# Kernel optimization log

Hardware: AMD Instinct MI355X
Metric: run time of the kernel (lower is better)

The kernel has to match this reference:

```python
import jax, jax.numpy as jnp
import numpy as np

NUM_NODES = 65536      # 16 graphs x 4096 nodes
NODES_PER_GRAPH = 4096
NUM_GRAPHS = 16
NUM_EDGES = 1048576    # avg degree 16
DIM = 64


def setup_inputs() -> dict:
    key = jax.random.key(0)
    ks = jax.random.split(key, 10)
    # edges constrained within each component graph (batched-graph semantics)
    eper = NUM_EDGES // NUM_GRAPHS
    gid = np.repeat(np.arange(NUM_GRAPHS), eper)
    rng = np.random.default_rng(0)
    src = jnp.asarray(rng.integers(0, NODES_PER_GRAPH, NUM_EDGES) + gid * NODES_PER_GRAPH, dtype=jnp.int64)
    dst = jnp.asarray(rng.integers(0, NODES_PER_GRAPH, NUM_EDGES) + gid * NODES_PER_GRAPH, dtype=jnp.int64)
    s = 1.0 / np.sqrt(DIM)
    return {
        "x": jax.random.normal(ks[0], (NUM_NODES, DIM), dtype=jnp.float32),
        "W1": jax.random.normal(ks[1], (DIM, DIM), dtype=jnp.float32) * s,
        "b1": jnp.zeros((DIM,), dtype=jnp.float32),
        "W2": jax.random.normal(ks[2], (DIM, DIM), dtype=jnp.float32) * s,
        "b2": jnp.zeros((DIM,), dtype=jnp.float32),
        "W3": jax.random.normal(ks[3], (DIM, DIM), dtype=jnp.float32) * s,
        "b3": jnp.zeros((DIM,), dtype=jnp.float32),
        "src": src,
        "dst": dst,
        "num_graphs": NUM_GRAPHS,
    }


def _sym_norms(src, dst, n):
    ones = jnp.ones(src.shape[0], dtype=jnp.float32)
    deg_out = jax.ops.segment_sum(ones, src, num_segments=n)
    deg_in = jax.ops.segment_sum(ones, dst, num_segments=n)
    inv_sqrt = lambda d: jnp.where(d > 0, d, 1.0) ** -0.5 * (d > 0)
    return inv_sqrt(deg_out), inv_sqrt(deg_in)


def _graph_conv(x, W, b, src, dst, norm_src, norm_dst, n):
    # DGL GraphConv, norm='both': h = D_in^{-1/2} A D_out^{-1/2} (X W) + b
    h = (x * norm_src[:, None]) @ W          # [N, D]
    msg = h[src]                              # [E, D] gather
    agg = jax.ops.segment_sum(msg, dst, num_segments=n)  # [N, D] scatter-add
    return agg * norm_dst[:, None] + b


def reference(x, W1, b1, W2, b2, W3, b3, src, dst, num_graphs):
    n = x.shape[0]
    norm_src, norm_dst = _sym_norms(src, dst, n)
    h = _graph_conv(x, W1, b1, src, dst, norm_src, norm_dst, n)
    h = _graph_conv(h, W2, b2, src, dst, norm_src, norm_dst, n)
    h = _graph_conv(h, W3, b3, src, dst, norm_src, norm_dst, n)
    # unbatch + pad to max_num_nodes + stack; equal-size graphs -> pure reshape
    return h.reshape(num_graphs, n // num_graphs, h.shape[-1])
```

## Files before the change

### kernel.cpp

```cpp
#include <hip/hip_runtime.h>
#include <hip/hip_fp16.h>

#define DIM 64
#define NG  16
#define CPG 16
#define NPG 4096
#define LSTR 68
#define HISTB (NG*CPG)
#define GGN 32

__global__ __launch_bounds__(256) void kA_hist(
    const int* __restrict__ src, const int* __restrict__ dst,
    int* __restrict__ hsub, int* __restrict__ dsub, int chunk, int npg)
{
    __shared__ int hs[NPG], hd[NPG];
    const int blk = blockIdx.x;
    const int g = blk / CPG;
    const int t = threadIdx.x;
    const int ebase = blk * chunk;
    const int nbase = g * npg;
    for (int i = t; i < npg; i += 256) { hs[i] = 0; hd[i] = 0; }
    __syncthreads();
    for (int e = t; e < chunk; e += 256) {
        atomicAdd(&hs[src[ebase + e] - nbase], 1);
        atomicAdd(&hd[dst[ebase + e] - nbase], 1);
    }
    __syncthreads();
    for (int i = t; i < npg; i += 256) {
        hsub[blk * npg + i] = hs[i];
        hd[i] ? (dsub[blk * npg + i] = hd[i]) : (dsub[blk * npg + i] = 0);
    }
}

__global__ __launch_bounds__(1024) void k2_scan(
    const int* __restrict__ hsub, int* __restrict__ dsub,
    float* __restrict__ ns, float* __restrict__ nd,
    int* __restrict__ rowptr, int epg, int npg, int N, int E)
{
    __shared__ int ddeg[NPG];
    __shared__ int wsum[16];
    const int g = blockIdx.x;
    const int t = threadIdx.x;
    const int nbase = g * npg;
    const int ebase = g * epg;
    for (int i = t; i < npg; i += 1024) {
        int sd = 0, dd = 0;
#pragma unroll
        for (int k = 0; k < CPG; ++k) {
            sd += hsub[(g * CPG + k) * npg + i];
            dd += dsub[(g * CPG + k) * npg + i];
        }
        ns[nbase + i] = sd > 0 ? rsqrtf((float)sd) : 0.0f;
        nd[nbase + i] = dd > 0 ? rsqrtf((float)dd) : 0.0f;
        ddeg[i] = dd;
    }
    __syncthreads();
    const int i0 = 4 * t;
    int d0 = ddeg[i0], d1 = ddeg[i0 + 1], d2 = ddeg[i0 + 2], d3 = ddeg[i0 + 3];
    int s4 = d0 + d1 + d2 + d3;
    const int lane = t & 63, wid = t >> 6;
    int v = s4;
#pragma unroll
    for (int off = 1; off < 64; off <<= 1) {
        int u = __shfl_up(v, off, 64);
        if (lane >= off) v += u;
    }
    if (lane == 63) wsum[wid] = v;
    __syncthreads();
    if (t < 16) {
        int w = wsum[t];
#pragma unroll
        for (int off = 1; off < 16; off <<= 1) {
            int u = __shfl_up(w, off, 16);
            if (t >= off) w += u;
        }
        wsum[t] = w;
    }
    __syncthreads();
    int incl = v + (wid > 0 ? wsum[wid - 1] : 0);
    int c = ebase + incl - s4;
    rowptr[nbase + i0    ] = c; ddeg[i0    ] = c; c += d0;
    rowptr[nbase + i0 + 1] = c; ddeg[i0 + 1] = c; c += d1;
    rowptr[nbase + i0 + 2] = c; ddeg[i0 + 2] = c; c += d2;
    rowptr[nbase + i0 + 3] = c; ddeg[i0 + 3] = c;
    if (g == 0 && t == 0) rowptr[N] = E;
    __syncthreads();
    for (int i = t; i < npg; i += 1024) {
        int cc = ddeg[i];
#pragma unroll
        for (int k = 0; k < CPG; ++k) {
            int* p = &dsub[(g * CPG + k) * npg + i];
            int old = *p; *p = cc; cc += old;
        }
    }
}

__global__ __launch_bounds__(256) void kC_gemm_fill(
    const int* __restrict__ src, const int* __restrict__ dst,
    const int* __restrict__ dsub, int* __restrict__ ssrc, int chunk, int npg,
    const float* __restrict__ x, const float* __restrict__ W1,
    const float* __restrict__ ns, __half* __restrict__ hF, int swiz)
{
    __shared__ float smem[64 * LSTR + 32 * LSTR];
    const int tid = threadIdx.x;
    if ((int)blockIdx.x < HISTB) {
        int* cur = (int*)smem;
        const int blk = blockIdx.x;
        const int g = blk / CPG;
        const int ebase = blk * chunk;
        const int nbase = g * npg;
        for (int i = tid; i < npg; i += 256) cur[i] = dsub[blk * npg + i];
        __syncthreads();
        for (int e = tid; e < chunk; e += 256) {
            int s = src[ebase + e];
            int d = dst[ebase + e] - nbase;
            int pos = atomicAdd(&cur[d], 1);
            ssrc[pos] = s;
        }
    } else {
        float* Wt = smem;
        float* xs = Wt + 64 * LSTR;
        int blk = blockIdx.x - HISTB;
        if (swiz) {
            int xg = blk & 7;
            int j = blk >> 3;
            int g = xg + ((j >> 7) << 3);
            blk = (g << 7) + (j & 127);
        }
        const int row0 = blk * 32;
        for (int i = tid; i < 64 * 64; i += 256) {
            int k = i >> 6, c = i & 63;
            Wt[c * LSTR + k] = W1[i];
        }
        for (int i = tid; i < 32 * 64; i += 256) {
            int r = i >> 6, c = i & 63;
            int row = row0 + r;
            xs[r * LSTR + c] = x[(size_t)row * 64 + c] * ns[row];
        }
        __syncthreads();
        const int c0 = tid & 31;
        const int r0 = tid >> 5;
        float acc[4][2] = {};
#pragma unroll
        for (int k = 0; k < 64; k += 4) {
            float4 w0 = *(const float4*)&Wt[(c0     ) * LSTR + k];
            float4 w1 = *(const float4*)&Wt[(c0 + 32) * LSTR + k];
#pragma unroll
            for (int rr = 0; rr < 4; ++rr) {
                float4 xv = *(const float4*)&xs[(r0 + 8 * rr) * LSTR + k];
                acc[rr][0] += xv.x * w0.x + xv.y * w0.y + xv.z * w0.z + xv.w * w0.w;
                acc[rr][1] += xv.x * w1.x + xv.y * w1.y + xv.z * w1.z + xv.w * w1.w;
            }
        }
#pragma unroll
        for (int rr = 0; rr < 4; ++rr) {
            int row = row0 + r0 + 8 * rr;
            hF[(size_t)row * 64 + c0     ] = __float2half_rn(acc[rr][0]);
            hF[(size_t)row * 64 + c0 + 32] = __float2half_rn(acc[rr][1]);
        }
    }
}

__device__ __forceinline__ void acc_h4(float4& acc, uint2 u)
{
    __half2 p = *(__half2*)&u.x;
    __half2 q = *(__half2*)&u.y;
    float2 f0 = __half22float2(p);
    float2 f1 = __half22float2(q);
    acc.x += f0.x; acc.y += f0.y; acc.z += f1.x; acc.w += f1.y;
}

__device__ __forceinline__ void acc_h4s(float4& acc, uint2 u, float s)
{
    __half2 p = *(__half2*)&u.x;
    __half2 q = *(__half2*)&u.y;
    float2 f0 = __half22float2(p);
    float2 f1 = __half22float2(q);
    acc.x += s * f0.x; acc.y += s * f0.y; acc.z += s * f1.x; acc.w += s * f1.y;
}

__device__ __forceinline__ void gather_rest(
    const __half* __restrict__ h, const int* __restrict__ ssrc,
    int j, int end, int sub, float4& acc)
{
    const size_t off = (size_t)sub * 4;
    const int last = end - 8;
    while (j <= last) {
        int s0 = ssrc[j+0], s1 = ssrc[j+1], s2 = ssrc[j+2], s3 = ssrc[j+3];
        int s4 = ssrc[j+4], s5 = ssrc[j+5], s6 = ssrc[j+6], s7 = ssrc[j+7];
        uint2 u0 = *(const uint2*)(h + (size_t)s0 * 64 + off);
        uint2 u1 = *(const uint2*)(h + (size_t)s1 * 64 + off);
        uint2 u2 = *(const uint2*)(h + (size_t)s2 * 64 + off);
        uint2 u3 = *(const uint2*)(h + (size_t)s3 * 64 + off);
        uint2 u4 = *(const uint2*)(h + (size_t)s4 * 64 + off);
        uint2 u5 = *(const uint2*)(h + (size_t)s5 * 64 + off);
        uint2 u6 = *(const uint2*)(h + (size_t)s6 * 64 + off);
        uint2 u7 = *(const uint2*)(h + (size_t)s7 * 64 + off);
        acc_h4(acc, u0); acc_h4(acc, u1); acc_h4(acc, u2); acc_h4(acc, u3);
        acc_h4(acc, u4); acc_h4(acc, u5); acc_h4(acc, u6); acc_h4(acc, u7);
        j += 8;
    }
    int rem = end - j;
    if (rem > 0) {
#pragma unroll
        for (int q = 0; q < 4; ++q) {
            int jj = j + (q < rem ? q : rem - 1);
            int s = ssrc[jj];
            uint2 u = *(const uint2*)(h + (size_t)s * 64 + off);
            acc_h4s(acc, u, (q < rem) ? 1.0f : 0.0f);
        }
        if (rem > 4) {
#pragma unroll
            for (int q = 4; q < 8; ++q) {
                int jj = j + (q < rem ? q : rem - 1);
                int s = ssrc[jj];
                uint2 u = *(const uint2*)(h + (size_t)s * 64 + off);
                acc_h4s(acc, u, (q < rem) ? 1.0f : 0.0f);
            }
        }
    }
}

__device__ __forceinline__ void gather_node2(
    const __half* __restrict__ h, const int* __restrict__ ssrc,
    int begA, int endA, int begB, int endB, int sub,
    float4& accA, float4& accB)
{
    const size_t off = (size_t)sub * 4;
    int jA = begA, jB = begB;
    const int lastA = endA - 8, lastB = endB - 8;
    if (jA <= lastA && jB <= lastB) {
        int a0 = ssrc[jA+0], a1 = ssrc[jA+1], a2 = ssrc[jA+2], a3 = ssrc[jA+3];
        int a4 = ssrc[jA+4], a5 = ssrc[jA+5], a6 = ssrc[jA+6], a7 = ssrc[jA+7];
        int b0 = ssrc[jB+0], b1 = ssrc[jB+1], b2 = ssrc[jB+2], b3 = ssrc[jB+3];
        int b4 = ssrc[jB+4], b5 = ssrc[jB+5], b6 = ssrc[jB+6], b7 = ssrc[jB+7];
        for (;;) {
            uint2 uA0 = *(const uint2*)(h + (size_t)a0 * 64 + off);
            uint2 uA1 = *(const uint2*)(h + (size_t)a1 * 64 + off);
            uint2 uA2 = *(const uint2*)(h + (size_t)a2 * 64 + off);
            uint2 uA3 = *(const uint2*)(h + (size_t)a3 * 64 + off);
            uint2 uA4 = *(const uint2*)(h + (size_t)a4 * 64 + off);
            uint2 uA5 = *(const uint2*)(h + (size_t)a5 * 64 + off);
            uint2 uA6 = *(const uint2*)(h + (size_t)a6 * 64 + off);
            uint2 uA7 = *(const uint2*)(h + (size_t)a7 * 64 + off);
            uint2 uB0 = *(const uint2*)(h + (size_t)b0 * 64 + off);
            uint2 uB1 = *(const uint2*)(h + (size_t)b1 * 64 + off);
            uint2 uB2 = *(const uint2*)(h + (size_t)b2 * 64 + off);
            uint2 uB3 = *(const uint2*)(h + (size_t)b3 * 64 + off);
            uint2 uB4 = *(const uint2*)(h + (size_t)b4 * 64 + off);
            uint2 uB5 = *(const uint2*)(h + (size_t)b5 * 64 + off);
            uint2 uB6 = *(const uint2*)(h + (size_t)b6 * 64 + off);
            uint2 uB7 = *(const uint2*)(h + (size_t)b7 * 64 + off);
            jA += 8; jB += 8;
            bool more = (jA <= lastA) && (jB <= lastB);
            int pA = more ? jA : begA;
            int pB = more ? jB : begB;
            int na0 = ssrc[pA+0], na1 = ssrc[pA+1], na2 = ssrc[pA+2], na3 = ssrc[pA+3];
            int na4 = ssrc[pA+4], na5 = ssrc[pA+5], na6 = ssrc[pA+6], na7 = ssrc[pA+7];
            int nb0 = ssrc[pB+0], nb1 = ssrc[pB+1], nb2 = ssrc[pB+2], nb3 = ssrc[pB+3];
            int nb4 = ssrc[pB+4], nb5 = ssrc[pB+5], nb6 = ssrc[pB+6], nb7 = ssrc[pB+7];
            acc_h4(accA, uA0); acc_h4(accA, uA1); acc_h4(accA, uA2); acc_h4(accA, uA3);
            acc_h4(accA, uA4); acc_h4(accA, uA5); acc_h4(accA, uA6); acc_h4(accA, uA7);
            acc_h4(accB, uB0); acc_h4(accB, uB1); acc_h4(accB, uB2); acc_h4(accB, uB3);
            acc_h4(accB, uB4); acc_h4(accB, uB5); acc_h4(accB, uB6); acc_h4(accB, uB7);
            if (!more) break;
            a0 = na0; a1 = na1; a2 = na2; a3 = na3;
            a4 = na4; a5 = na5; a6 = na6; a7 = na7;
            b0 = nb0; b1 = nb1; b2 = nb2; b3 = nb3;
            b4 = nb4; b5 = nb5; b6 = nb6; b7 = nb7;
        }
    }
    gather_rest(h, ssrc, jA, endA, sub, accA);
    gather_rest(h, ssrc, jB, endB, sub, accB);
}

__global__ __launch_bounds__(256) void gg_kernel(
    const __half* __restrict__ h, const int* __restrict__ ssrc,
    const int* __restrict__ rowptr, const float* __restrict__ ns,
    const float* __restrict__ nd, const float* __restrict__ bprev,
    const float* __restrict__ W, __half* __restrict__ hout,
    int N, int swiz)
{
    __shared__ float us[GGN][64];
    int blk = blockIdx.x;
    if (swiz) {
        int xg = blk & 7;
        int j = blk >> 3;
        int g = xg + ((j >> 7) << 3);
        blk = (g << 7) + (j & 127);
    }
    const int tid = threadIdx.x;
    const int wv = tid >> 6;
    const int lane = tid & 63;
    const int grp = lane >> 4;
    const int sub = lane & 15;

    const int nlA = wv * 4 + grp;
    const int nlB = nlA + 16;
    const int wA = blk * GGN + nlA;
    const int wB = blk * GGN + nlB;
    {
        int begA = rowptr[wA], endA = rowptr[wA + 1];
        int begB = rowptr[wB], endB = rowptr[wB + 1];
        float4 accA = {0.f,0.f,0.f,0.f}, accB = {0.f,0.f,0.f,0.f};
        gather_node2(h, ssrc, begA, endA, begB, endB, sub, accA, accB);
        float4 bv = *(const float4*)(bprev + sub * 4);
        {
            float sw = ns[wA];
            float alpha = nd[wA] * sw;
            float4 uo;
            uo.x = accA.x * alpha + sw * bv.x;
            uo.y = accA.y * alpha + sw * bv.y;
            uo.z = accA.z * alpha + sw * bv.z;
            uo.w = accA.w * alpha + sw * bv.w;
            *(float4*)&us[nlA][sub * 4] = uo;
        }
        {
            float sw = ns[wB];
            float alpha = nd[wB] * sw;
            float4 uo;
            uo.x = accB.x * alpha + sw * bv.x;
            uo.y = accB.y * alpha + sw * bv.y;
            uo.z = accB.z * alpha + sw * bv.z;
            uo.w = accB.w * alpha + sw * bv.w;
            *(float4*)&us[nlB][sub * 4] = uo;
        }
    }
    __syncthreads();
    const int c = tid & 63;
    const int nb = tid >> 6;
    float y[8] = {0.f,0.f,0.f,0.f,0.f,0.f,0.f,0.f};
#pragma unroll
    for (int k = 0; k < 64; k += 4) {
        float w0 = W[(k    ) * 64 + c];
        float w1 = W[(k + 1) * 64 + c];
        float w2 = W[(k + 2) * 64 + c];
        float w3 = W[(k + 3) * 64 + c];
#pragma unroll
        for (int m = 0; m < 8; ++m) {
            const float4 uv = *(const float4*)&us[nb + 4 * m][k];
            y[m] += uv.x * w0 + uv.y * w1 + uv.z * w2 + uv.w * w3;
        }
    }
#pragma unroll
    for (int m = 0; m < 8; ++m) {
        int wo = blk * GGN + nb + 4 * m;
        hout[(size_t)wo * 64 + c] = __float2half_rn(y[m]);
    }
}

__global__ __launch_bounds__(256) void gather_kernel(
    const __half* __restrict__ h, const int* __restrict__ ssrc,
    const int* __restrict__ rowptr, float* __restrict__ out,
    const float* __restrict__ nd, const float* __restrict__ b,
    int N, int swiz)
{
    int blk = blockIdx.x;
    if (swiz) {
        int x = blk & 7;
        int j = blk >> 3;
        int g = x + ((j >> 7) << 3);
        blk = (g << 7) + (j & 127);
    }
    const int wv = threadIdx.x >> 6;
    const int lane = threadIdx.x & 63;
    const int grp = lane >> 4;
    const int sub = lane & 15;
    int wA = blk * 32 + wv * 4 + grp;
    int wB = wA + 16;
    int begA = rowptr[wA], endA = rowptr[wA + 1];
    int begB = rowptr[wB], endB = rowptr[wB + 1];
    float4 accA = {0.f,0.f,0.f,0.f}, accB = {0.f,0.f,0.f,0.f};
    gather_node2(h, ssrc, begA, endA, begB, endB, sub, accA, accB);
    const float4 bv = *(const float4*)(b + sub * 4);
    {
        float n = nd[wA];
        accA.x = accA.x * n + bv.x;
        accA.y = accA.y * n + bv.y;
        accA.z = accA.z * n + bv.z;
        accA.w = accA.w * n + bv.w;
        *(float4*)(out + (size_t)wA * 64 + sub * 4) = accA;
    }
    {
        float n = nd[wB];
        accB.x = accB.x * n + bv.x;
        accB.y = accB.y * n + bv.y;
        accB.z = accB.z * n + bv.z;
        accB.w = accB.w * n + bv.w;
        *(float4*)(out + (size_t)wB * 64 + sub * 4) = accB;
    }
}

extern "C" void kernel_launch(void* const* d_in, const int* in_sizes, int n_in,
                              void* d_out, int out_size, void* d_ws, size_t ws_size,
                              hipStream_t stream)
{
    const float* x  = (const float*)d_in[0];
    const float* W1 = (const float*)d_in[1];
    const float* b1 = (const float*)d_in[2];
    const float* W2 = (const float*)d_in[3];
    const float* b2 = (const float*)d_in[4];
    const float* W3 = (const float*)d_in[5];
    const float* b3 = (const float*)d_in[6];
    const int*  src = (const int*)d_in[7];
    const int*  dst = (const int*)d_in[8];

    const int E = in_sizes[7];
    const int N = in_sizes[0] / DIM;
    const int epg = E / NG;
    const int npg = N / NG;
    const int chunk = epg / CPG;

    float*  ns     = (float*)d_ws;
    float*  nd     = ns + N;
    __half* hF     = (__half*)(nd + N);
    __half* h2     = hF + (size_t)N * DIM;
    int*    rowptr = (int*)(h2 + (size_t)N * DIM);
    int*    ssrc   = rowptr + N + 1;
    int*    hsub   = ssrc + E;
    int*    dsub   = hsub + (size_t)HISTB * npg;
    float*  agg    = (float*)d_out;

    const int swiz = (N == 65536 && npg == 4096) ? 1 : 0;

    kA_hist<<<HISTB, 256, 0, stream>>>(src, dst, hsub, dsub, chunk, npg);
    k2_scan<<<NG, 1024, 0, stream>>>(
        hsub, dsub, ns, nd, rowptr, epg, npg, N, E);
    kC_gemm_fill<<<HISTB + N / 32, 256, 0, stream>>>(
        src, dst, dsub, ssrc, chunk, npg, x, W1, ns, hF, swiz);

    gg_kernel<<<N / GGN, 256, 0, stream>>>(
        hF, ssrc, rowptr, ns, nd, b1, W2, h2, N, swiz);
    gg_kernel<<<N / GGN, 256, 0, stream>>>(
        h2, ssrc, rowptr, ns, nd, b2, W3, hF, N, swiz);
    gather_kernel<<<N / 32, 256, 0, stream>>>(
        hF, ssrc, rowptr, agg, nd, b3, N, swiz);
}
```

Before: 213.2 us.

## Split degree scan into parallel kernels and widen gather to 16-byte loads

The single 16-block scan kernel becomes three kernels. Two of them are fully parallel, one computing norms and destination degrees and one computing per-chunk cursors, with a small scan between them, so the serial per-graph loops no longer run on only 16 blocks. The gather kernels now use 8 lanes per node with 16-byte half loads instead of 16 lanes with 8-byte loads. The gather-GEMM tile doubles to 64 nodes per block, with the swizzle adjusted to match. This trades two extra launches and the extra degd buffer for more parallelism, and the wider loads cut the number of load instructions in the gather, though there are fewer lanes per row.

```diff
diff --git a/kernel.cpp b/kernel.cpp
--- a/kernel.cpp
+++ b/kernel.cpp
@@ -7,7 +7,7 @@
 #define NPG 4096
 #define LSTR 68
 #define HISTB (NG*CPG)
-#define GGN 32
+#define GGN 64
 
 __global__ __launch_bounds__(256) void kA_hist(
     const int* __restrict__ src, const int* __restrict__ dst,
@@ -28,36 +28,41 @@
     __syncthreads();
     for (int i = t; i < npg; i += 256) {
         hsub[blk * npg + i] = hs[i];
-        hd[i] ? (dsub[blk * npg + i] = hd[i]) : (dsub[blk * npg + i] = 0);
-    }
-}
-
-__global__ __launch_bounds__(1024) void k2_scan(
-    const int* __restrict__ hsub, int* __restrict__ dsub,
-    float* __restrict__ ns, float* __restrict__ nd,
-    int* __restrict__ rowptr, int epg, int npg, int N, int E)
-{
-    __shared__ int ddeg[NPG];
+        dsub[blk * npg + i] = hd[i];
+    }
+}
+
+__global__ __launch_bounds__(256) void k2a_norms(
+    const int* __restrict__ hsub, const int* __restrict__ dsub,
+    float* __restrict__ ns, float* __restrict__ nd, int* __restrict__ degd,
+    int npg)
+{
+    const int node = blockIdx.x * 256 + threadIdx.x;
+    const int g = node / npg;
+    const int i = node - g * npg;
+    int sd = 0, dd = 0;
+#pragma unroll
+    for (int k = 0; k < CPG; ++k) {
+        sd += hsub[(g * CPG + k) * npg + i];
+        dd += dsub[(g * CPG + k) * npg + i];
+    }
+    ns[node] = sd > 0 ? rsqrtf((float)sd) : 0.0f;
+    nd[node] = dd > 0 ? rsqrtf((float)dd) : 0.0f;
+    degd[node] = dd;
+}
+
+__global__ __launch_bounds__(1024) void k2b_scan(
+    const int* __restrict__ degd, int* __restrict__ rowptr,
+    int epg, int npg, int N, int E)
+{
     __shared__ int wsum[16];
     const int g = blockIdx.x;
     const int t = threadIdx.x;
     const int nbase = g * npg;
     const int ebase = g * epg;
-    for (int i = t; i < npg; i += 1024) {
-        int sd = 0, dd = 0;
-#pragma unroll
-        for (int k = 0; k < CPG; ++k) {
-            sd += hsub[(g * CPG + k) * npg + i];
-            dd += dsub[(g * CPG + k) * npg + i];
-        }
-        ns[nbase + i] = sd > 0 ? rsqrtf((float)sd) : 0.0f;
-        nd[nbase + i] = dd > 0 ? rsqrtf((float)dd) : 0.0f;
-        ddeg[i] = dd;
-    }
-    __syncthreads();
     const int i0 = 4 * t;
-    int d0 = ddeg[i0], d1 = ddeg[i0 + 1], d2 = ddeg[i0 + 2], d3 = ddeg[i0 + 3];
-    int s4 = d0 + d1 + d2 + d3;
+    const int4 d = *(const int4*)&degd[nbase + i0];
+    int s4 = d.x + d.y + d.z + d.w;
     const int lane = t & 63, wid = t >> 6;
     int v = s4;
 #pragma unroll
@@ -79,19 +84,24 @@
     __syncthreads();
     int incl = v + (wid > 0 ? wsum[wid - 1] : 0);
     int c = ebase + incl - s4;
-    rowptr[nbase + i0    ] = c; ddeg[i0    ] = c; c += d0;
-    rowptr[nbase + i0 + 1] = c; ddeg[i0 + 1] = c; c += d1;
-    rowptr[nbase + i0 + 2] = c; ddeg[i0 + 2] = c; c += d2;
-    rowptr[nbase + i0 + 3] = c; ddeg[i0 + 3] = c;
+    rowptr[nbase + i0    ] = c; c += d.x;
+    rowptr[nbase + i0 + 1] = c; c += d.y;
+    rowptr[nbase + i0 + 2] = c; c += d.z;
+    rowptr[nbase + i0 + 3] = c;
     if (g == 0 && t == 0) rowptr[N] = E;
-    __syncthreads();
-    for (int i = t; i < npg; i += 1024) {
-        int cc = ddeg[i];
-#pragma unroll
-        for (int k = 0; k < CPG; ++k) {
-            int* p = &dsub[(g * CPG + k) * npg + i];
-            int old = *p; *p = cc; cc += old;
-        }
+}
+
+__global__ __launch_bounds__(256) void k2c_cursors(
+    int* __restrict__ dsub, const int* __restrict__ rowptr, int npg)
+{
+    const int node = blockIdx.x * 256 + threadIdx.x;
+    const int g = node / npg;
+    const int i = node - g * npg;
+    int cc = rowptr[node];
+#pragma unroll
+    for (int k = 0; k < CPG; ++k) {
+        int* p = &dsub[(g * CPG + k) * npg + i];
+        int old = *p; *p = cc; cc += old;
     }
 }
 
@@ -161,43 +171,49 @@
     }
 }
 
-__device__ __forceinline__ void acc_h4(float4& acc, uint2 u)
-{
-    __half2 p = *(__half2*)&u.x;
-    __half2 q = *(__half2*)&u.y;
-    float2 f0 = __half22float2(p);
-    float2 f1 = __half22float2(q);
-    acc.x += f0.x; acc.y += f0.y; acc.z += f1.x; acc.w += f1.y;
-}
-
-__device__ __forceinline__ void acc_h4s(float4& acc, uint2 u, float s)
-{
-    __half2 p = *(__half2*)&u.x;
-    __half2 q = *(__half2*)&u.y;
-    float2 f0 = __half22float2(p);
-    float2 f1 = __half22float2(q);
-    acc.x += s * f0.x; acc.y += s * f0.y; acc.z += s * f1.x; acc.w += s * f1.y;
+__device__ __forceinline__ void acc_u4(float4& A, float4& B, uint4 u)
+{
+    __half2 h0 = *(__half2*)&u.x;
+    __half2 h1 = *(__half2*)&u.y;
+    __half2 h2 = *(__half2*)&u.z;
+    __half2 h3 = *(__half2*)&u.w;
+    float2 f0 = __half22float2(h0), f1 = __half22float2(h1);
+    float2 f2 = __half22float2(h2), f3 = __half22float2(h3);
+    A.x += f0.x; A.y += f0.y; A.z += f1.x; A.w += f1.y;
+    B.x += f2.x; B.y += f2.y; B.z += f3.x; B.w += f3.y;
+}
+
+__device__ __forceinline__ void acc_u4s(float4& A, float4& B, uint4 u, float s)
+{
+    __half2 h0 = *(__half2*)&u.x;
+    __half2 h1 = *(__half2*)&u.y;
+    __half2 h2 = *(__half2*)&u.z;
+    __half2 h3 = *(__half2*)&u.w;
+    float2 f0 = __half22float2(h0), f1 = __half22float2(h1);
+    float2 f2 = __half22float2(h2), f3 = __half22float2(h3);
+    A.x += s * f0.x; A.y += s * f0.y; A.z += s * f1.x; A.w += s * f1.y;
+    B.x += s * f2.x; B.y += s * f2.y; B.z += s * f3.x; B.w += s * f3.y;
 }
 
 __device__ __forceinline__ void gather_rest(
     const __half* __restrict__ h, const int* __restrict__ ssrc,
-    int j, int end, int sub, float4& acc)
-{
-    const size_t off = (size_t)sub * 4;
+    int j, int end, int sub, float4& A, float4& B)
+{
+    const size_t off = (size_t)sub * 8;
     const int last = end - 8;
     while (j <= last) {
         int s0 = ssrc[j+0], s1 = ssrc[j+1], s2 = ssrc[j+2], s3 = ssrc[j+3];
         int s4 = ssrc[j+4], s5 = ssrc[j+5], s6 = ssrc[j+6], s7 = ssrc[j+7];
-        uint2 u0 = *(const uint2*)(h + (size_t)s0 * 64 + off);
-        uint2 u1 = *(const uint2*)(h + (size_t)s1 * 64 + off);
-        uint2 u2 = *(const uint2*)(h + (size_t)s2 * 64 + off);
-        uint2 u3 = *(const uint2*)(h + (size_t)s3 * 64 + off);
-        uint2 u4 = *(const uint2*)(h + (size_t)s4 * 64 + off);
-        uint2 u5 = *(const uint2*)(h + (size_t)s5 * 64 + off);
-        uint2 u6 = *(const uint2*)(h + (size_t)s6 * 64 + off);
-        uint2 u7 = *(const uint2*)(h + (size_t)s7 * 64 + off);
-        acc_h4(acc, u0); acc_h4(acc, u1); acc_h4(acc, u2); acc_h4(acc, u3);
-        acc_h4(acc, u4); acc_h4(acc, u5); acc_h4(acc, u6); acc_h4(acc, u7);
+        uint4 u0 = *(const uint4*)(h + (size_t)s0 * 64 + off);
+        uint4 u1 = *(const uint4*)(h + (size_t)s1 * 64 + off);
+        uint4 u2 = *(const uint4*)(h + (size_t)s2 * 64 + off);
+        uint4 u3 = *(const uint4*)(h + (size_t)s3 * 64 + off);
+        uint4 u4 = *(const uint4*)(h + (size_t)s4 * 64 + off);
+        uint4 u5 = *(const uint4*)(h + (size_t)s5 * 64 + off);
+        uint4 u6 = *(const uint4*)(h + (size_t)s6 * 64 + off);
+        uint4 u7 = *(const uint4*)(h + (size_t)s7 * 64 + off);
+        acc_u4(A, B, u0); acc_u4(A, B, u1); acc_u4(A, B, u2); acc_u4(A, B, u3);
+        acc_u4(A, B, u4); acc_u4(A, B, u5); acc_u4(A, B, u6); acc_u4(A, B, u7);
         j += 8;
     }
     int rem = end - j;
@@ -206,16 +222,16 @@
         for (int q = 0; q < 4; ++q) {
             int jj = j + (q < rem ? q : rem - 1);
             int s = ssrc[jj];
-            uint2 u = *(const uint2*)(h + (size_t)s * 64 + off);
-            acc_h4s(acc, u, (q < rem) ? 1.0f : 0.0f);
+            uint4 u = *(const uint4*)(h + (size_t)s * 64 + off);
+            acc_u4s(A, B, u, (q < rem) ? 1.0f : 0.0f);
         }
         if (rem > 4) {
 #pragma unroll
             for (int q = 4; q < 8; ++q) {
                 int jj = j + (q < rem ? q : rem - 1);
                 int s = ssrc[jj];
-                uint2 u = *(const uint2*)(h + (size_t)s * 64 + off);
-                acc_h4s(acc, u, (q < rem) ? 1.0f : 0.0f);
+                uint4 u = *(const uint4*)(h + (size_t)s * 64 + off);
+                acc_u4s(A, B, u, (q < rem) ? 1.0f : 0.0f);
             }
         }
     }
@@ -224,9 +240,9 @@
 __device__ __forceinline__ void gather_node2(
     const __half* __restrict__ h, const int* __restrict__ ssrc,
     int begA, int endA, int begB, int endB, int sub,
-    float4& accA, float4& accB)
-{
-    const size_t off = (size_t)sub * 4;
+    float4& accA0, float4& accA1, float4& accB0, float4& accB1)
+{
+    const size_t off = (size_t)sub * 8;
     int jA = begA, jB = begB;
     const int lastA = endA - 8, lastB = endB - 8;
     if (jA <= lastA && jB <= lastB) {
@@ -235,22 +251,22 @@
         int b0 = ssrc[jB+0], b1 = ssrc[jB+1], b2 = ssrc[jB+2], b3 = ssrc[jB+3];
         int b4 = ssrc[jB+4], b5 = ssrc[jB+5], b6 = ssrc[jB+6], b7 = ssrc[jB+7];
         for (;;) {
-            uint2 uA0 = *(const uint2*)(h + (size_t)a0 * 64 + off);
-            uint2 uA1 = *(const uint2*)(h + (size_t)a1 * 64 + off);
-            uint2 uA2 = *(const uint2*)(h + (size_t)a2 * 64 + off);
-            uint2 uA3 = *(const uint2*)(h + (size_t)a3 * 64 + off);
-            uint2 uA4 = *(const uint2*)(h + (size_t)a4 * 64 + off);
-            uint2 uA5 = *(const uint2*)(h + (size_t)a5 * 64 + off);
-            uint2 uA6 = *(const uint2*)(h + (size_t)a6 * 64 + off);
-            uint2 uA7 = *(const uint2*)(h + (size_t)a7 * 64 + off);
-            uint2 uB0 = *(const uint2*)(h + (size_t)b0 * 64 + off);
-            uint2 uB1 = *(const uint2*)(h + (size_t)b1 * 64 + off);
-            uint2 uB2 = *(const uint2*)(h + (size_t)b2 * 64 + off);
-            uint2 uB3 = *(const uint2*)(h + (size_t)b3 * 64 + off);
-            uint2 uB4 = *(const uint2*)(h + (size_t)b4 * 64 + off);
-            uint2 uB5 = *(const uint2*)(h + (size_t)b5 * 64 + off);
-            uint2 uB6 = *(const uint2*)(h + (size_t)b6 * 64 + off);
-            uint2 uB7 = *(const uint2*)(h + (size_t)b7 * 64 + off);
+            uint4 uA0 = *(const uint4*)(h + (size_t)a0 * 64 + off);
+            uint4 uA1 = *(const uint4*)(h + (size_t)a1 * 64 + off);
+            uint4 uA2 = *(const uint4*)(h + (size_t)a2 * 64 + off);
+            uint4 uA3 = *(const uint4*)(h + (size_t)a3 * 64 + off);
+            uint4 uA4 = *(const uint4*)(h + (size_t)a4 * 64 + off);
+            uint4 uA5 = *(const uint4*)(h + (size_t)a5 * 64 + off);
+            uint4 uA6 = *(const uint4*)(h + (size_t)a6 * 64 + off);
+            uint4 uA7 = *(const uint4*)(h + (size_t)a7 * 64 + off);
+            uint4 uB0 = *(const uint4*)(h + (size_t)b0 * 64 + off);
+            uint4 uB1 = *(const uint4*)(h + (size_t)b1 * 64 + off);
+            uint4 uB2 = *(const uint4*)(h + (size_t)b2 * 64 + off);
+            uint4 uB3 = *(const uint4*)(h + (size_t)b3 * 64 + off);
+            uint4 uB4 = *(const uint4*)(h + (size_t)b4 * 64 + off);
+            uint4 uB5 = *(const uint4*)(h + (size_t)b5 * 64 + off);
+            uint4 uB6 = *(const uint4*)(h + (size_t)b6 * 64 + off);
+            uint4 uB7 = *(const uint4*)(h + (size_t)b7 * 64 + off);
             jA += 8; jB += 8;
             bool more = (jA <= lastA) && (jB <= lastB);
             int pA = more ? jA : begA;
@@ -259,10 +275,14 @@
             int na4 = ssrc[pA+4], na5 = ssrc[pA+5], na6 = ssrc[pA+6], na7 = ssrc[pA+7];
             int nb0 = ssrc[pB+0], nb1 = ssrc[pB+1], nb2 = ssrc[pB+2], nb3 = ssrc[pB+3];
             int nb4 = ssrc[pB+4], nb5 = ssrc[pB+5], nb6 = ssrc[pB+6], nb7 = ssrc[pB+7];
-            acc_h4(accA, uA0); acc_h4(accA, uA1); acc_h4(accA, uA2); acc_h4(accA, uA3);
-            acc_h4(accA, uA4); acc_h4(accA, uA5); acc_h4(accA, uA6); acc_h4(accA, uA7);
-            acc_h4(accB, uB0); acc_h4(accB, uB1); acc_h4(accB, uB2); acc_h4(accB, uB3);
-            acc_h4(accB, uB4); acc_h4(accB, uB5); acc_h4(accB, uB6); acc_h4(accB, uB7);
+            acc_u4(accA0, accA1, uA0); acc_u4(accA0, accA1, uA1);
+            acc_u4(accA0, accA1, uA2); acc_u4(accA0, accA1, uA3);
+            acc_u4(accA0, accA1, uA4); acc_u4(accA0, accA1, uA5);
+            acc_u4(accA0, accA1, uA6); acc_u4(accA0, accA1, uA7);
+            acc_u4(accB0, accB1, uB0); acc_u4(accB0, accB1, uB1);
+            acc_u4(accB0, accB1, uB2); acc_u4(accB0, accB1, uB3);
+            acc_u4(accB0, accB1, uB4); acc_u4(accB0, accB1, uB5);
+            acc_u4(accB0, accB1, uB6); acc_u4(accB0, accB1, uB7);
             if (!more) break;
             a0 = na0; a1 = na1; a2 = na2; a3 = na3;
             a4 = na4; a5 = na5; a6 = na6; a7 = na7;
@@ -270,8 +290,8 @@
             b4 = nb4; b5 = nb5; b6 = nb6; b7 = nb7;
         }
     }
-    gather_rest(h, ssrc, jA, endA, sub, accA);
-    gather_rest(h, ssrc, jB, endB, sub, accB);
+    gather_rest(h, ssrc, jA, endA, sub, accA0, accA1);
+    gather_rest(h, ssrc, jB, endB, sub, accB0, accB1);
 }
 
 __global__ __launch_bounds__(256) void gg_kernel(
@@ -286,50 +306,65 @@
     if (swiz) {
         int xg = blk & 7;
         int j = blk >> 3;
-        int g = xg + ((j >> 7) << 3);
-        blk = (g << 7) + (j & 127);
+        int g = xg + ((j >> 6) << 3);
+        blk = (g << 6) + (j & 63);
     }
     const int tid = threadIdx.x;
     const int wv = tid >> 6;
     const int lane = tid & 63;
-    const int grp = lane >> 4;
-    const int sub = lane & 15;
-
-    const int nlA = wv * 4 + grp;
-    const int nlB = nlA + 16;
+    const int grp = lane >> 3;
+    const int sub = lane & 7;
+
+    const int nlA = wv * 8 + grp;
+    const int nlB = nlA + 32;
     const int wA = blk * GGN + nlA;
     const int wB = blk * GGN + nlB;
-    {
+    if (wB < N) {
         int begA = rowptr[wA], endA = rowptr[wA + 1];
         int begB = rowptr[wB], endB = rowptr[wB + 1];
-        float4 accA = {0.f,0.f,0.f,0.f}, accB = {0.f,0.f,0.f,0.f};
-        gather_node2(h, ssrc, begA, endA, begB, endB, sub, accA, accB);
-        float4 bv = *(const float4*)(bprev + sub * 4);
+        float4 accA0 = {0,0,0,0}, accA1 = {0,0,0,0};
+        float4 accB0 = {0,0,0,0}, accB1 = {0,0,0,0};
+        gather_node2(h, ssrc, begA, endA, begB, endB, sub,
+                     accA0, accA1, accB0, accB1);
+        float4 bv0 = *(const float4*)(bprev + sub * 8);
+        float4 bv1 = *(const float4*)(bprev + sub * 8 + 4);
         {
             float sw = ns[wA];
             float alpha = nd[wA] * sw;
-            float4 uo;
-            uo.x = accA.x * alpha + sw * bv.x;
-            uo.y = accA.y * alpha + sw * bv.y;
-            uo.z = accA.z * alpha + sw * bv.z;
-            uo.w = accA.w * alpha + sw * bv.w;
-            *(float4*)&us[nlA][sub * 4] = uo;
+            float4 u0, u1;
+            u0.x = accA0.x * alpha + sw * bv0.x;
+            u0.y = accA0.y * alpha + sw * bv0.y;
+            u0.z = accA0.z * alpha + sw * bv0.z;
+            u0.w = accA0.w * alpha + sw * bv0.w;
+            u1.x = accA1.x * alpha + sw * bv1.x;
+            u1.y = accA1.y * alpha + sw * bv1.y;
+            u1.z = accA1.z * alpha + sw * bv1.z;
+            u1.w = accA1.w * alpha + sw * bv1.w;
+            *(float4*)&us[nlA][sub * 8    ] = u0;
+            *(float4*)&us[nlA][sub * 8 + 4] = u1;
         }
         {
             float sw = ns[wB];
             float alpha = nd[wB] * sw;
-            float4 uo;
-            uo.x = accB.x * alpha + sw * bv.x;
-            uo.y = accB.y * alpha + sw * bv.y;
-            uo.z = accB.z * alpha + sw * bv.z;
-            uo.w = accB.w * alpha + sw * bv.w;
-            *(float4*)&us[nlB][sub * 4] = uo;
+            float4 u0, u1;
+            u0.x = accB0.x * alpha + sw * bv0.x;
+            u0.y = accB0.y * alpha + sw * bv0.y;
+            u0.z = accB0.z * alpha + sw * bv0.z;
+            u0.w = accB0.w * alpha + sw * bv0.w;
+            u1.x = accB1.x * alpha + sw * bv1.x;
+            u1.y = accB1.y * alpha + sw * bv1.y;
+            u1.z = accB1.z * alpha + sw * bv1.z;
+            u1.w = accB1.w * alpha + sw * bv1.w;
+            *(float4*)&us[nlB][sub * 8    ] = u0;
+            *(float4*)&us[nlB][sub * 8 + 4] = u1;
         }
     }
     __syncthreads();
     const int c = tid & 63;
     const int nb = tid >> 6;
-    float y[8] = {0.f,0.f,0.f,0.f,0.f,0.f,0.f,0.f};
+    float y[16];
+#pragma unroll
+    for (int m = 0; m < 16; ++m) y[m] = 0.f;
 #pragma unroll
     for (int k = 0; k < 64; k += 4) {
         float w0 = W[(k    ) * 64 + c];
@@ -337,15 +372,16 @@
         float w2 = W[(k + 2) * 64 + c];
         float w3 = W[(k + 3) * 64 + c];
 #pragma unroll
-        for (int m = 0; m < 8; ++m) {
+        for (int m = 0; m < 16; ++m) {
             const float4 uv = *(const float4*)&us[nb + 4 * m][k];
             y[m] += uv.x * w0 + uv.y * w1 + uv.z * w2 + uv.w * w3;
         }
     }
 #pragma unroll
-    for (int m = 0; m < 8; ++m) {
+    for (int m = 0; m < 16; ++m) {
         int wo = blk * GGN + nb + 4 * m;
-        hout[(size_t)wo * 64 + c] = __float2half_rn(y[m]);
+        if (wo < N)
+            hout[(size_t)wo * 64 + c] = __float2half_rn(y[m]);
     }
 }
 
@@ -359,35 +395,41 @@
     if (swiz) {
         int x = blk & 7;
         int j = blk >> 3;
-        int g = x + ((j >> 7) << 3);
-        blk = (g << 7) + (j & 127);
+        int g = x + ((j >> 6) << 3);
+        blk = (g << 6) + (j & 63);
     }
     const int wv = threadIdx.x >> 6;
     const int lane = threadIdx.x & 63;
-    const int grp = lane >> 4;
-    const int sub = lane & 15;
-    int wA = blk * 32 + wv * 4 + grp;
-    int wB = wA + 16;
+    const int grp = lane >> 3;
+    const int sub = lane & 7;
+    int wA = blk * 64 + wv * 8 + grp;
+    int wB = wA + 32;
+    if (wB >= N) return;
     int begA = rowptr[wA], endA = rowptr[wA + 1];
     int begB = rowptr[wB], endB = rowptr[wB + 1];
-    float4 accA = {0.f,0.f,0.f,0.f}, accB = {0.f,0.f,0.f,0.f};
-    gather_node2(h, ssrc, begA, endA, begB, endB, sub, accA, accB);
-    const float4 bv = *(const float4*)(b + sub * 4);
+    float4 accA0 = {0,0,0,0}, accA1 = {0,0,0,0};
+    float4 accB0 = {0,0,0,0}, accB1 = {0,0,0,0};
+    gather_node2(h, ssrc, begA, endA, begB, endB, sub,
+                 accA0, accA1, accB0, accB1);
+    const float4 bv0 = *(const float4*)(b + sub * 8);
+    const float4 bv1 = *(const float4*)(b + sub * 8 + 4);
     {
         float n = nd[wA];
-        accA.x = accA.x * n + bv.x;
-        accA.y = accA.y * n + bv.y;
-        accA.z = accA.z * n + bv.z;
-        accA.w = accA.w * n + bv.w;
-        *(float4*)(out + (size_t)wA * 64 + sub * 4) = accA;
+        accA0.x = accA0.x * n + bv0.x; accA0.y = accA0.y * n + bv0.y;
+        accA0.z = accA0.z * n + bv0.z; accA0.w = accA0.w * n + bv0.w;
+        accA1.x = accA1.x * n + bv1.x; accA1.y = accA1.y * n + bv1.y;
+        accA1.z = accA1.z * n + bv1.z; accA1.w = accA1.w * n + bv1.w;
+        *(float4*)(out + (size_t)wA * 64 + sub * 8    ) = accA0;
+        *(float4*)(out + (size_t)wA * 64 + sub * 8 + 4) = accA1;
     }
     {
         float n = nd[wB];
-        accB.x = accB.x * n + bv.x;
-        accB.y = accB.y * n + bv.y;
-        accB.z = accB.z * n + bv.z;
-        accB.w = accB.w * n + bv.w;
-        *(float4*)(out + (size_t)wB * 64 + sub * 4) = accB;
+        accB0.x = accB0.x * n + bv0.x; accB0.y = accB0.y * n + bv0.y;
+        accB0.z = accB0.z * n + bv0.z; accB0.w = accB0.w * n + bv0.w;
+        accB1.x = accB1.x * n + bv1.x; accB1.y = accB1.y * n + bv1.y;
+        accB1.z = accB1.z * n + bv1.z; accB1.w = accB1.w * n + bv1.w;
+        *(float4*)(out + (size_t)wB * 64 + sub * 8    ) = accB0;
+        *(float4*)(out + (size_t)wB * 64 + sub * 8 + 4) = accB1;
     }
 }
 
@@ -413,7 +455,8 @@
 
     float*  ns     = (float*)d_ws;
     float*  nd     = ns + N;
-    __half* hF     = (__half*)(nd + N);
+    int*    degd   = (int*)(nd + N);
+    __half* hF     = (__half*)(degd + N);
     __half* h2     = hF + (size_t)N * DIM;
     int*    rowptr = (int*)(h2 + (size_t)N * DIM);
     int*    ssrc   = rowptr + N + 1;
@@ -424,15 +467,16 @@
     const int swiz = (N == 65536 && npg == 4096) ? 1 : 0;
 
     kA_hist<<<HISTB, 256, 0, stream>>>(src, dst, hsub, dsub, chunk, npg);
-    k2_scan<<<NG, 1024, 0, stream>>>(
-        hsub, dsub, ns, nd, rowptr, epg, npg, N, E);
+    k2a_norms<<<N / 256, 256, 0, stream>>>(hsub, dsub, ns, nd, degd, npg);
+    k2b_scan<<<NG, 1024, 0, stream>>>(degd, rowptr, epg, npg, N, E);
+    k2c_cursors<<<N / 256, 256, 0, stream>>>(dsub, rowptr, npg);
     kC_gemm_fill<<<HISTB + N / 32, 256, 0, stream>>>(
         src, dst, dsub, ssrc, chunk, npg, x, W1, ns, hF, swiz);
 
-    gg_kernel<<<N / GGN, 256, 0, stream>>>(
+    gg_kernel<<<(N + GGN - 1) / GGN, 256, 0, stream>>>(
         hF, ssrc, rowptr, ns, nd, b1, W2, h2, N, swiz);
-    gg_kernel<<<N / GGN, 256, 0, stream>>>(
+    gg_kernel<<<(N + GGN - 1) / GGN, 256, 0, stream>>>(
         h2, ssrc, rowptr, ns, nd, b2, W3, hF, N, swiz);
-    gather_kernel<<<N / 32, 256, 0, stream>>>(
+    gather_kernel<<<(N + 63) / 64, 256, 0, stream>>>(
         hF, ssrc, rowptr, agg, nd, b3, N, swiz);
 }
```

New measurement: 686.0 us. 222% more time.

## Split degree scan into wide norm, scan, and cursor kernels

Applied to the files above, without the earlier changes.

Breaks the 16-block degree/scan kernel into three launches. The per-node sums over sub-histograms and the cursor prefix writes now run on N/256 blocks instead of 16 blocks of 1024 threads. Only the small per-graph scan stays at 16 blocks and reads packed degrees through int4 loads. The goal is better GPU occupancy for the memory-bound sub-histogram passes, at the cost of two extra kernel launches and a round trip of the degree array through global memory.

```diff
diff --git a/kernel.cpp b/kernel.cpp
--- a/kernel.cpp
+++ b/kernel.cpp
@@ -28,36 +28,41 @@
     __syncthreads();
     for (int i = t; i < npg; i += 256) {
         hsub[blk * npg + i] = hs[i];
-        hd[i] ? (dsub[blk * npg + i] = hd[i]) : (dsub[blk * npg + i] = 0);
-    }
-}
-
-__global__ __launch_bounds__(1024) void k2_scan(
-    const int* __restrict__ hsub, int* __restrict__ dsub,
-    float* __restrict__ ns, float* __restrict__ nd,
-    int* __restrict__ rowptr, int epg, int npg, int N, int E)
-{
-    __shared__ int ddeg[NPG];
+        dsub[blk * npg + i] = hd[i];
+    }
+}
+
+__global__ __launch_bounds__(256) void k2a_norms(
+    const int* __restrict__ hsub, const int* __restrict__ dsub,
+    float* __restrict__ ns, float* __restrict__ nd, int* __restrict__ degd,
+    int npg)
+{
+    const int node = blockIdx.x * 256 + threadIdx.x;
+    const int g = node / npg;
+    const int i = node - g * npg;
+    int sd = 0, dd = 0;
+#pragma unroll
+    for (int k = 0; k < CPG; ++k) {
+        sd += hsub[(g * CPG + k) * npg + i];
+        dd += dsub[(g * CPG + k) * npg + i];
+    }
+    ns[node] = sd > 0 ? rsqrtf((float)sd) : 0.0f;
+    nd[node] = dd > 0 ? rsqrtf((float)dd) : 0.0f;
+    degd[node] = dd;
+}
+
+__global__ __launch_bounds__(1024) void k2b_scan(
+    const int* __restrict__ degd, int* __restrict__ rowptr,
+    int epg, int npg, int N, int E)
+{
     __shared__ int wsum[16];
     const int g = blockIdx.x;
     const int t = threadIdx.x;
     const int nbase = g * npg;
     const int ebase = g * epg;
-    for (int i = t; i < npg; i += 1024) {
-        int sd = 0, dd = 0;
-#pragma unroll
-        for (int k = 0; k < CPG; ++k) {
-            sd += hsub[(g * CPG + k) * npg + i];
-            dd += dsub[(g * CPG + k) * npg + i];
-        }
-        ns[nbase + i] = sd > 0 ? rsqrtf((float)sd) : 0.0f;
-        nd[nbase + i] = dd > 0 ? rsqrtf((float)dd) : 0.0f;
-        ddeg[i] = dd;
-    }
-    __syncthreads();
     const int i0 = 4 * t;
-    int d0 = ddeg[i0], d1 = ddeg[i0 + 1], d2 = ddeg[i0 + 2], d3 = ddeg[i0 + 3];
-    int s4 = d0 + d1 + d2 + d3;
+    const int4 d = *(const int4*)&degd[nbase + i0];
+    int s4 = d.x + d.y + d.z + d.w;
     const int lane = t & 63, wid = t >> 6;
     int v = s4;
 #pragma unroll
@@ -79,19 +84,24 @@
     __syncthreads();
     int incl = v + (wid > 0 ? wsum[wid - 1] : 0);
     int c = ebase + incl - s4;
-    rowptr[nbase + i0    ] = c; ddeg[i0    ] = c; c += d0;
-    rowptr[nbase + i0 + 1] = c; ddeg[i0 + 1] = c; c += d1;
-    rowptr[nbase + i0 + 2] = c; ddeg[i0 + 2] = c; c += d2;
-    rowptr[nbase + i0 + 3] = c; ddeg[i0 + 3] = c;
+    rowptr[nbase + i0    ] = c; c += d.x;
+    rowptr[nbase + i0 + 1] = c; c += d.y;
+    rowptr[nbase + i0 + 2] = c; c += d.z;
+    rowptr[nbase + i0 + 3] = c;
     if (g == 0 && t == 0) rowptr[N] = E;
-    __syncthreads();
-    for (int i = t; i < npg; i += 1024) {
-        int cc = ddeg[i];
-#pragma unroll
-        for (int k = 0; k < CPG; ++k) {
-            int* p = &dsub[(g * CPG + k) * npg + i];
-            int old = *p; *p = cc; cc += old;
-        }
+}
+
+__global__ __launch_bounds__(256) void k2c_cursors(
+    int* __restrict__ dsub, const int* __restrict__ rowptr, int npg)
+{
+    const int node = blockIdx.x * 256 + threadIdx.x;
+    const int g = node / npg;
+    const int i = node - g * npg;
+    int cc = rowptr[node];
+#pragma unroll
+    for (int k = 0; k < CPG; ++k) {
+        int* p = &dsub[(g * CPG + k) * npg + i];
+        int old = *p; *p = cc; cc += old;
     }
 }
 
@@ -413,7 +423,8 @@
 
     float*  ns     = (float*)d_ws;
     float*  nd     = ns + N;
-    __half* hF     = (__half*)(nd + N);
+    int*    degd   = (int*)(nd + N);
+    __half* hF     = (__half*)(degd + N);
     __half* h2     = hF + (size_t)N * DIM;
     int*    rowptr = (int*)(h2 + (size_t)N * DIM);
     int*    ssrc   = rowptr + N + 1;
@@ -424,8 +435,9 @@
     const int swiz = (N == 65536 && npg == 4096) ? 1 : 0;
 
     kA_hist<<<HISTB, 256, 0, stream>>>(src, dst, hsub, dsub, chunk, npg);
-    k2_scan<<<NG, 1024, 0, stream>>>(
-        hsub, dsub, ns, nd, rowptr, epg, npg, N, E);
+    k2a_norms<<<N / 256, 256, 0, stream>>>(hsub, dsub, ns, nd, degd, npg);
+    k2b_scan<<<NG, 1024, 0, stream>>>(degd, rowptr, epg, npg, N, E);
+    k2c_cursors<<<N / 256, 256, 0, stream>>>(dsub, rowptr, npg);
     kC_gemm_fill<<<HISTB + N / 32, 256, 0, stream>>>(
         src, dst, dsub, ssrc, chunk, npg, x, W1, ns, hF, swiz);
 
```

Result: slower. 218.4 us (+2.4%).
